# Kernel optimization log

Measured on AMD Instinct MI355X. Metric: run time of the kernel, lower is better.

The kernel has to match this reference:

```python
import jax, jax.numpy as jnp
import numpy as np

D = 1024
H = 16
DK = D // H
TB = 64  # temporal_bias_dim
SCALE = DK ** -0.5


def setup_inputs() -> dict:
    key = jax.random.key(0)
    ks = jax.random.split(key, 12)
    B, S = 8, 512
    s = 0.02
    return {
        "x": jax.random.normal(ks[0], (B, S, D), jnp.float32),
        "padding_masks": jnp.ones((B, 1, 1, S), jnp.int32),
        "batch_temporal_mat": jax.random.uniform(ks[1], (B, S, S), jnp.float32) * 100.0,
        "wq": jax.random.normal(ks[2], (D, D), jnp.float32) * s,
        "bq": jnp.zeros((D,), jnp.float32),
        "wk": jax.random.normal(ks[3], (D, D), jnp.float32) * s,
        "bk": jnp.zeros((D,), jnp.float32),
        "wv": jax.random.normal(ks[4], (D, D), jnp.float32) * s,
        "bv": jnp.zeros((D,), jnp.float32),
        "w_proj": jax.random.normal(ks[5], (D, D), jnp.float32) * s,
        "b_proj": jnp.zeros((D,), jnp.float32),
        "w_tb1": jax.random.normal(ks[6], (1, TB), jnp.float32) * 0.5,
        "b_tb1": jnp.zeros((TB,), jnp.float32),
        "w_tb2": jax.random.normal(ks[7], (TB, 1), jnp.float32) * 0.5,
        "b_tb2": jnp.zeros((1,), jnp.float32),
    }


def reference(x, padding_masks, batch_temporal_mat, wq, bq, wk, bk, wv, bv,
              w_proj, b_proj, w_tb1, b_tb1, w_tb2, b_tb2):
    B, S, _ = x.shape

    def heads(w, b):
        return (x @ w + b).reshape(B, S, H, DK).transpose(0, 2, 1, 3)  # (B,H,S,DK)

    q, k, v = heads(wq, bq), heads(wk, bk), heads(wv, bv)
    scores = jnp.einsum("bhqd,bhkd->bhqk", q, k) * SCALE  # (B,H,S,S)

    # temporal bias: 1/log(e + t) -> Linear(1,64) -> leaky_relu(0.2) -> Linear(64,1)
    t = 1.0 / jnp.log(jnp.exp(jnp.float32(1.0)) + batch_temporal_mat)  # (B,S,S)
    h = t[..., None] * w_tb1[0] + b_tb1  # (B,S,S,TB)
    h = jnp.where(h >= 0, h, 0.2 * h)
    bias = (h @ w_tb2)[..., 0] + b_tb2[0]  # (B,S,S)
    scores = scores + bias[:, None, :, :]

    neg_inf = jnp.float32(-jnp.inf)
    scores = jnp.where(padding_masks == 0, neg_inf, scores)
    causal = jnp.triu(jnp.ones((S, S), bool), k=1)  # (S,S), add_cls=False
    scores = jnp.where(causal[None, None], neg_inf, scores)

    p_attn = jax.nn.softmax(scores, axis=-1)
    out = jnp.einsum("bhqk,bhkd->bhqd", p_attn, v)
    out = out.transpose(0, 2, 1, 3).reshape(B, S, D)
    out = out @ w_proj + b_proj
    return out
```

## Files before the change

kernel.cpp:

```cpp
#include <hip/hip_runtime.h>
#include <hip/hip_bf16.h>

#define B_  8
#define S_  512
#define D_  1024
#define H_  16
#define DK_ 64
#define TB_ 64
#define SCALE_ 0.125f

typedef __attribute__((ext_vector_type(8))) short          bh8;
typedef __attribute__((ext_vector_type(4))) float          f32x4;
typedef __attribute__((ext_vector_type(8))) unsigned short us8;

__device__ __forceinline__ unsigned short f2bf(float f) {
    unsigned u = __float_as_uint(f);
    unsigned r = 0x7fffu + ((u >> 16) & 1u);
    return (unsigned short)((u + r) >> 16);
}

__global__ __launch_bounds__(256)
void cvt_x_kernel(const float* __restrict__ in, unsigned short* __restrict__ out, int n8)
{
    int i = blockIdx.x * 256 + threadIdx.x;
    if (i >= n8) return;
    float4 a = *(const float4*)&in[(size_t)i * 8];
    float4 b = *(const float4*)&in[(size_t)i * 8 + 4];
    us8 o;
    o[0] = f2bf(a.x); o[1] = f2bf(a.y); o[2] = f2bf(a.z); o[3] = f2bf(a.w);
    o[4] = f2bf(b.x); o[5] = f2bf(b.y); o[6] = f2bf(b.z); o[7] = f2bf(b.w);
    *(us8*)&out[(size_t)i * 8] = o;
}

__global__ __launch_bounds__(256)
void cvt_wt_kernel(const float* __restrict__ W, unsigned short* __restrict__ Wt)
{
    __shared__ float t[64][65];
    const int bx = blockIdx.x, by = blockIdx.y;
    const int c  = threadIdx.x & 63;
    const int r0 = threadIdx.x >> 6;
    #pragma unroll
    for (int i = 0; i < 16; ++i) {
        int r = r0 + i * 4;
        t[r][c] = W[(size_t)(by * 64 + r) * 1024 + bx * 64 + c];
    }
    __syncthreads();
    #pragma unroll
    for (int i = 0; i < 16; ++i) {
        int r = r0 + i * 4;
        Wt[(size_t)(bx * 64 + r) * 1024 + by * 64 + c] = f2bf(t[c][r]);
    }
}

template<int MODE>
__global__ __launch_bounds__(256)
void gemm_bf16_kernel(const unsigned short* __restrict__ A,
                      const unsigned short* __restrict__ Bt,
                      const float* __restrict__ bias,
                      float* __restrict__ C, unsigned short* __restrict__ Cb)
{
    __shared__ unsigned short As[128][72];
    __shared__ unsigned short Bs[128][72];
    const int tid  = threadIdx.x;
    const int lane = tid & 63;
    const int wid  = tid >> 6;
    const int wr   = wid >> 1, wc = wid & 1;
    const int row0 = blockIdx.x * 128;
    const int col0 = blockIdx.y * 128;

    f32x4 acc[4][4] = {};

    const int ur = tid >> 3;
    const int uc = (tid & 7) * 8;
    const int fr = lane & 15;
    const int fk = (lane >> 4) * 8;

    for (int k0 = 0; k0 < 1024; k0 += 64) {
        __syncthreads();
        #pragma unroll
        for (int i = 0; i < 4; ++i) {
            int r = ur + i * 32;
            *(int4*)&As[r][uc] = *(const int4*)&A [(size_t)(row0 + r) * 1024 + k0 + uc];
            *(int4*)&Bs[r][uc] = *(const int4*)&Bt[(size_t)(col0 + r) * 1024 + k0 + uc];
        }
        __syncthreads();
        #pragma unroll
        for (int ks = 0; ks < 2; ++ks) {
            bh8 af[4], bfr[4];
            #pragma unroll
            for (int r = 0; r < 4; ++r)
                af[r]  = *(const bh8*)&As[wr * 64 + r * 16 + fr][ks * 32 + fk];
            #pragma unroll
            for (int c = 0; c < 4; ++c)
                bfr[c] = *(const bh8*)&Bs[wc * 64 + c * 16 + fr][ks * 32 + fk];
            #pragma unroll
            for (int r = 0; r < 4; ++r)
                #pragma unroll
                for (int c = 0; c < 4; ++c)
                    acc[r][c] = __builtin_amdgcn_mfma_f32_16x16x32_bf16(
                        af[r], bfr[c], acc[r][c], 0, 0, 0);
        }
    }

    #pragma unroll
    for (int r = 0; r < 4; ++r) {
        #pragma unroll
        for (int c = 0; c < 4; ++c) {
            int n = col0 + wc * 64 + c * 16 + (lane & 15);
            float bn = bias[n];
            #pragma unroll
            for (int j = 0; j < 4; ++j) {
                int m = row0 + wr * 64 + r * 16 + (lane >> 4) * 4 + j;
                float o = acc[r][c][j] + bn;
                if (MODE == 0) {
                    C[(size_t)m * 1024 + n] = o;
                } else {
                    int bb = m >> 9, ss = m & 511;
                    int hh = n >> 6, dd = n & 63;
                    if (MODE == 1)
                        Cb[((size_t)((bb * H_ + hh) * S_ + ss)) * DK_ + dd] = f2bf(o);
                    else
                        Cb[((size_t)((bb * H_ + hh) * DK_ + dd)) * S_ + ss] = f2bf(o);
                }
            }
        }
    }
}

__global__ __launch_bounds__(256)
void tbias_kernel(const float* __restrict__ tm, const int* __restrict__ pmask,
                  const float* __restrict__ w1, const float* __restrict__ b1,
                  const float* __restrict__ w2, const float* __restrict__ b2,
                  float* __restrict__ bias)
{
    __shared__ float sw1[TB_], sb1[TB_], sw2[TB_];
    if (threadIdx.x < TB_) {
        sw1[threadIdx.x] = w1[threadIdx.x];
        sb1[threadIdx.x] = b1[threadIdx.x];
        sw2[threadIdx.x] = w2[threadIdx.x];
    }
    __syncthreads();
    const float ec  = 2.7182818284590452f;
    const float b2v = b2[0];
    const int n = B_ * S_ * S_;
    for (int i = blockIdx.x * blockDim.x + threadIdx.x; i < n;
         i += gridDim.x * blockDim.x) {
        int bb = i >> 18;
        int jj = i & (S_ - 1);
        float t   = 1.0f / logf(ec + tm[i]);
        float acc = b2v;
        #pragma unroll
        for (int j = 0; j < TB_; ++j) {
            float h = fmaf(t, sw1[j], sb1[j]);
            h = (h >= 0.f) ? h : 0.2f * h;
            acc = fmaf(h, sw2[j], acc);
        }
        bias[i] = (pmask[bb * S_ + jj] == 0) ? -1e30f : acc;
    }
}

__global__ __launch_bounds__(256)
void attn_kernel(const unsigned short* __restrict__ q,
                 const unsigned short* __restrict__ k,
                 const unsigned short* __restrict__ vt,
                 const float* __restrict__ biasm,
                 unsigned short* __restrict__ outb)
{
    __shared__ unsigned short Kl[64][72];
    __shared__ unsigned short Vl[64][72];
    __shared__ unsigned short Pl[64][72];

    const int tid  = threadIdx.x;
    const int lane = tid & 63;
    const int w    = tid >> 6;
    const int qt   = blockIdx.x;
    const int h    = blockIdx.y;
    const int b    = blockIdx.z;
    const int q0   = qt * 64;

    const int l15 = lane & 15;
    const int g   = lane >> 4;

    const size_t hb  = (size_t)(b * H_ + h) * S_;
    const unsigned short* kbase  = k  + hb * DK_;
    const unsigned short* vtbase = vt + ((size_t)(b * H_ + h) * DK_) * S_;

    const int qrow_a = q0 + w * 16 + l15;
    bh8 aq0 = *(const bh8*)&q[(hb + qrow_a) * DK_ +      g * 8];
    bh8 aq1 = *(const bh8*)&q[(hb + qrow_a) * DK_ + 32 + g * 8];

    const int qd = q0 + w * 16 + g * 4;

    f32x4 acc_o[4] = {};
    float m_run[4] = { -1e30f, -1e30f, -1e30f, -1e30f };
    float l_run[4] = {};

    for (int kt = 0; kt <= qt; ++kt) {
        __syncthreads();
        #pragma unroll
        for (int s = 0; s < 2; ++s) {
            int u  = tid + s * 256;
            int r  = u >> 3;
            int c8 = (u & 7) * 8;
            *(int4*)&Kl[r][c8] = *(const int4*)&kbase [(size_t)(kt * 64 + r) * DK_ + c8];
            *(int4*)&Vl[r][c8] = *(const int4*)&vtbase[(size_t)r * S_ + kt * 64 + c8];
        }
        __syncthreads();

        f32x4 sc[4];
        #pragma unroll
        for (int c = 0; c < 4; ++c) {
            bh8 bk0 = *(const bh8*)&Kl[c * 16 + l15][     g * 8];
            bh8 bk1 = *(const bh8*)&Kl[c * 16 + l15][32 + g * 8];
            f32x4 z = {};
            z = __builtin_amdgcn_mfma_f32_16x16x32_bf16(aq0, bk0, z, 0, 0, 0);
            sc[c] = __builtin_amdgcn_mfma_f32_16x16x32_bf16(aq1, bk1, z, 0, 0, 0);
        }

        float sv[4][4];
        #pragma unroll
        for (int j = 0; j < 4; ++j) {
            const float* br = biasm + ((size_t)b * S_ + qd + j) * S_ + kt * 64;
            #pragma unroll
            for (int c = 0; c < 4; ++c)
                sv[c][j] = fmaf(sc[c][j], SCALE_, br[c * 16 + l15]);
        }
        if (kt == qt) {
            #pragma unroll
            for (int c = 0; c < 4; ++c) {
                int kloc = c * 16 + l15;
                #pragma unroll
                for (int j = 0; j < 4; ++j)
                    if (kloc > w * 16 + g * 4 + j) sv[c][j] = -1e30f;
            }
        }

        #pragma unroll
        for (int j = 0; j < 4; ++j) {
            float mt = fmaxf(fmaxf(sv[0][j], sv[1][j]), fmaxf(sv[2][j], sv[3][j]));
            mt = fmaxf(mt, __shfl_xor(mt, 1));
            mt = fmaxf(mt, __shfl_xor(mt, 2));
            mt = fmaxf(mt, __shfl_xor(mt, 4));
            mt = fmaxf(mt, __shfl_xor(mt, 8));
            float m_new = fmaxf(m_run[j], mt);
            float resc  = __expf(m_run[j] - m_new);
            float psum  = 0.f;
            #pragma unroll
            for (int c = 0; c < 4; ++c) {
                float p = __expf(sv[c][j] - m_new);
                Pl[w * 16 + g * 4 + j][c * 16 + l15] = f2bf(p);
                psum += p;
            }
            psum += __shfl_xor(psum, 1);
            psum += __shfl_xor(psum, 2);
            psum += __shfl_xor(psum, 4);
            psum += __shfl_xor(psum, 8);
            l_run[j] = l_run[j] * resc + psum;
            m_run[j] = m_new;
            acc_o[0][j] *= resc; acc_o[1][j] *= resc;
            acc_o[2][j] *= resc; acc_o[3][j] *= resc;
        }

        asm volatile("s_waitcnt lgkmcnt(0)" ::: "memory");

        bh8 ap0 = *(const bh8*)&Pl[w * 16 + l15][     g * 8];
        bh8 ap1 = *(const bh8*)&Pl[w * 16 + l15][32 + g * 8];
        #pragma unroll
        for (int c2 = 0; c2 < 4; ++c2) {
            bh8 bv0 = *(const bh8*)&Vl[c2 * 16 + l15][     g * 8];
            bh8 bv1 = *(const bh8*)&Vl[c2 * 16 + l15][32 + g * 8];
            acc_o[c2] = __builtin_amdgcn_mfma_f32_16x16x32_bf16(ap0, bv0, acc_o[c2], 0, 0, 0);
            acc_o[c2] = __builtin_amdgcn_mfma_f32_16x16x32_bf16(ap1, bv1, acc_o[c2], 0, 0, 0);
        }
    }

    #pragma unroll
    for (int j = 0; j < 4; ++j) {
        float linv = 1.f / l_run[j];
        #pragma unroll
        for (int c2 = 0; c2 < 4; ++c2)
            outb[((size_t)(b * S_ + qd + j)) * D_ + h * DK_ + c2 * 16 + l15] =
                f2bf(acc_o[c2][j] * linv);
    }
}

extern "C" void kernel_launch(void* const* d_in, const int* in_sizes, int n_in,
                              void* d_out, int out_size, void* d_ws, size_t ws_size,
                              hipStream_t stream)
{
    const float* x     = (const float*)d_in[0];
    const int*   pm    = (const int*)  d_in[1];
    const float* tm    = (const float*)d_in[2];
    const float* wq    = (const float*)d_in[3];
    const float* bq    = (const float*)d_in[4];
    const float* wk    = (const float*)d_in[5];
    const float* bk    = (const float*)d_in[6];
    const float* wv    = (const float*)d_in[7];
    const float* bv    = (const float*)d_in[8];
    const float* wp    = (const float*)d_in[9];
    const float* bp    = (const float*)d_in[10];
    const float* w_tb1 = (const float*)d_in[11];
    const float* b_tb1 = (const float*)d_in[12];
    const float* w_tb2 = (const float*)d_in[13];
    const float* b_tb2 = (const float*)d_in[14];

    char* wsb = (char*)d_ws;
    const size_t MB = 1u << 20;
    unsigned short* xb  = (unsigned short*)wsb;
    unsigned short* wtq = (unsigned short*)(wsb + 8  * MB);
    unsigned short* wtk = wtq + 1048576;
    unsigned short* wtv = wtk + 1048576;
    unsigned short* wtp = wtv + 1048576;
    unsigned short* qw  = (unsigned short*)(wsb + 16 * MB);
    unsigned short* kw  = (unsigned short*)(wsb + 24 * MB);
    unsigned short* vtw = (unsigned short*)(wsb + 32 * MB);
    float*          bw  = (float*)        (wsb + 40 * MB);

    cvt_x_kernel<<<2048, 256, 0, stream>>>(x, xb, 524288);
    dim3 gw(16, 16);
    cvt_wt_kernel<<<gw, 256, 0, stream>>>(wq, wtq);
    cvt_wt_kernel<<<gw, 256, 0, stream>>>(wk, wtk);
    cvt_wt_kernel<<<gw, 256, 0, stream>>>(wv, wtv);
    cvt_wt_kernel<<<gw, 256, 0, stream>>>(wp, wtp);

    dim3 gg(32, 8);
    gemm_bf16_kernel<1><<<gg, 256, 0, stream>>>(xb, wtq, bq, nullptr, qw);
    gemm_bf16_kernel<1><<<gg, 256, 0, stream>>>(xb, wtk, bk, nullptr, kw);
    gemm_bf16_kernel<2><<<gg, 256, 0, stream>>>(xb, wtv, bv, nullptr, vtw);

    tbias_kernel<<<2048, 256, 0, stream>>>(tm, pm, w_tb1, b_tb1, w_tb2, b_tb2, bw);

    dim3 ga(8, H_, B_);
    attn_kernel<<<ga, 256, 0, stream>>>(qw, kw, vtw, bw, xb );

    gemm_bf16_kernel<0><<<gg, 256, 0, stream>>>(xb, wtp, bp, (float*)d_out, nullptr);
}
```

Measured before the change: 262.9 us.

## Fuse QKV GEMMs into one launch, shrink GEMM tiles, remap attention blocks

The three Q/K/V projection GEMMs become a single launch over a concatenated transposed weight buffer. Each block picks its bias and output layout from its column range. GEMM tiles shrink from 128x128 to 128x64, so the QKV grid has 1536 blocks and the projection grid 512, which gives more blocks per CU on the many-CU device. The attention launch becomes a 1D grid with a swizzled block-to-(b,h,qt) mapping so that consecutive blocks land on different XCDs, which may improve L2 locality for K/V. The smaller tiles reload A more often in exchange for better occupancy and less wave quantisation.

```diff
diff --git a/kernel.cpp b/kernel.cpp
--- a/kernel.cpp
+++ b/kernel.cpp
@@ -52,76 +52,153 @@
     }
 }
 
-template<int MODE>
-__global__ __launch_bounds__(256)
-void gemm_bf16_kernel(const unsigned short* __restrict__ A,
-                      const unsigned short* __restrict__ Bt,
-                      const float* __restrict__ bias,
-                      float* __restrict__ C, unsigned short* __restrict__ Cb)
+__global__ __launch_bounds__(256)
+void gemm_qkv_kernel(const unsigned short* __restrict__ A,
+                     const unsigned short* __restrict__ Wt,
+                     const float* __restrict__ bq, const float* __restrict__ bk,
+                     const float* __restrict__ bv,
+                     unsigned short* __restrict__ qo,
+                     unsigned short* __restrict__ ko,
+                     unsigned short* __restrict__ vo)
 {
     __shared__ unsigned short As[128][72];
-    __shared__ unsigned short Bs[128][72];
+    __shared__ unsigned short Bs[64][72];
     const int tid  = threadIdx.x;
     const int lane = tid & 63;
     const int wid  = tid >> 6;
     const int wr   = wid >> 1, wc = wid & 1;
     const int row0 = blockIdx.x * 128;
-    const int col0 = blockIdx.y * 128;
-
-    f32x4 acc[4][4] = {};
+    const int col0 = blockIdx.y * 64;
+
+    f32x4 acc[4][2] = {};
 
     const int ur = tid >> 3;
     const int uc = (tid & 7) * 8;
     const int fr = lane & 15;
     const int fk = (lane >> 4) * 8;
+    const int g  = lane >> 4;
 
     for (int k0 = 0; k0 < 1024; k0 += 64) {
         __syncthreads();
         #pragma unroll
         for (int i = 0; i < 4; ++i) {
             int r = ur + i * 32;
-            *(int4*)&As[r][uc] = *(const int4*)&A [(size_t)(row0 + r) * 1024 + k0 + uc];
-            *(int4*)&Bs[r][uc] = *(const int4*)&Bt[(size_t)(col0 + r) * 1024 + k0 + uc];
+            *(int4*)&As[r][uc] = *(const int4*)&A[(size_t)(row0 + r) * 1024 + k0 + uc];
+        }
+        #pragma unroll
+        for (int i = 0; i < 2; ++i) {
+            int r = ur + i * 32;
+            *(int4*)&Bs[r][uc] = *(const int4*)&Wt[(size_t)(col0 + r) * 1024 + k0 + uc];
         }
         __syncthreads();
         #pragma unroll
         for (int ks = 0; ks < 2; ++ks) {
-            bh8 af[4], bfr[4];
+            bh8 af[4], bfr[2];
             #pragma unroll
             for (int r = 0; r < 4; ++r)
                 af[r]  = *(const bh8*)&As[wr * 64 + r * 16 + fr][ks * 32 + fk];
             #pragma unroll
-            for (int c = 0; c < 4; ++c)
-                bfr[c] = *(const bh8*)&Bs[wc * 64 + c * 16 + fr][ks * 32 + fk];
+            for (int c = 0; c < 2; ++c)
+                bfr[c] = *(const bh8*)&Bs[wc * 32 + c * 16 + fr][ks * 32 + fk];
             #pragma unroll
             for (int r = 0; r < 4; ++r)
                 #pragma unroll
-                for (int c = 0; c < 4; ++c)
+                for (int c = 0; c < 2; ++c)
                     acc[r][c] = __builtin_amdgcn_mfma_f32_16x16x32_bf16(
                         af[r], bfr[c], acc[r][c], 0, 0, 0);
         }
     }
 
+    const int nh = col0 >> 10;
+    const float* bsel = (nh == 0) ? bq : (nh == 1) ? bk : bv;
+    unsigned short* outp = (nh == 0) ? qo : (nh == 1) ? ko : vo;
+
     #pragma unroll
     for (int r = 0; r < 4; ++r) {
         #pragma unroll
-        for (int c = 0; c < 4; ++c) {
-            int n = col0 + wc * 64 + c * 16 + (lane & 15);
+        for (int c = 0; c < 2; ++c) {
+            int n  = col0 + wc * 32 + c * 16 + (lane & 15);
+            int nn = n & 1023;
+            float bn = bsel[nn];
+            int hh = nn >> 6, dd = nn & 63;
+            #pragma unroll
+            for (int j = 0; j < 4; ++j) {
+                int m = row0 + wr * 64 + r * 16 + g * 4 + j;
+                float o = acc[r][c][j] + bn;
+                int bb = m >> 9, ss = m & 511;
+                if (nh == 2)
+                    outp[((size_t)((bb * H_ + hh) * DK_ + dd)) * S_ + ss] = f2bf(o);
+                else
+                    outp[((size_t)((bb * H_ + hh) * S_ + ss)) * DK_ + dd] = f2bf(o);
+            }
+        }
+    }
+}
+
+__global__ __launch_bounds__(256)
+void gemm_proj_kernel(const unsigned short* __restrict__ A,
+                      const unsigned short* __restrict__ Wt,
+                      const float* __restrict__ bias,
+                      float* __restrict__ C)
+{
+    __shared__ unsigned short As[128][72];
+    __shared__ unsigned short Bs[64][72];
+    const int tid  = threadIdx.x;
+    const int lane = tid & 63;
+    const int wid  = tid >> 6;
+    const int wr   = wid >> 1, wc = wid & 1;
+    const int row0 = blockIdx.x * 128;
+    const int col0 = blockIdx.y * 64;
+
+    f32x4 acc[4][2] = {};
+
+    const int ur = tid >> 3;
+    const int uc = (tid & 7) * 8;
+    const int fr = lane & 15;
+    const int fk = (lane >> 4) * 8;
+    const int g  = lane >> 4;
+
+    for (int k0 = 0; k0 < 1024; k0 += 64) {
+        __syncthreads();
+        #pragma unroll
+        for (int i = 0; i < 4; ++i) {
+            int r = ur + i * 32;
+            *(int4*)&As[r][uc] = *(const int4*)&A[(size_t)(row0 + r) * 1024 + k0 + uc];
+        }
+        #pragma unroll
+        for (int i = 0; i < 2; ++i) {
+            int r = ur + i * 32;
+            *(int4*)&Bs[r][uc] = *(const int4*)&Wt[(size_t)(col0 + r) * 1024 + k0 + uc];
+        }
+        __syncthreads();
+        #pragma unroll
+        for (int ks = 0; ks < 2; ++ks) {
+            bh8 af[4], bfr[2];
+            #pragma unroll
+            for (int r = 0; r < 4; ++r)
+                af[r]  = *(const bh8*)&As[wr * 64 + r * 16 + fr][ks * 32 + fk];
+            #pragma unroll
+            for (int c = 0; c < 2; ++c)
+                bfr[c] = *(const bh8*)&Bs[wc * 32 + c * 16 + fr][ks * 32 + fk];
+            #pragma unroll
+            for (int r = 0; r < 4; ++r)
+                #pragma unroll
+                for (int c = 0; c < 2; ++c)
+                    acc[r][c] = __builtin_amdgcn_mfma_f32_16x16x32_bf16(
+                        af[r], bfr[c], acc[r][c], 0, 0, 0);
+        }
+    }
+
+    #pragma unroll
+    for (int r = 0; r < 4; ++r) {
+        #pragma unroll
+        for (int c = 0; c < 2; ++c) {
+            int n = col0 + wc * 32 + c * 16 + (lane & 15);
             float bn = bias[n];
             #pragma unroll
             for (int j = 0; j < 4; ++j) {
-                int m = row0 + wr * 64 + r * 16 + (lane >> 4) * 4 + j;
-                float o = acc[r][c][j] + bn;
-                if (MODE == 0) {
-                    C[(size_t)m * 1024 + n] = o;
-                } else {
-                    int bb = m >> 9, ss = m & 511;
-                    int hh = n >> 6, dd = n & 63;
-                    if (MODE == 1)
-                        Cb[((size_t)((bb * H_ + hh) * S_ + ss)) * DK_ + dd] = f2bf(o);
-                    else
-                        Cb[((size_t)((bb * H_ + hh) * DK_ + dd)) * S_ + ss] = f2bf(o);
-                }
+                int m = row0 + wr * 64 + r * 16 + g * 4 + j;
+                C[(size_t)m * 1024 + n] = acc[r][c][j] + bn;
             }
         }
     }
@@ -173,10 +250,11 @@
     const int tid  = threadIdx.x;
     const int lane = tid & 63;
     const int w    = tid >> 6;
-    const int qt   = blockIdx.x;
-    const int h    = blockIdx.y;
-    const int b    = blockIdx.z;
-    const int q0   = qt * 64;
+    const int lin = (blockIdx.x & 7) * 128 + (blockIdx.x >> 3);
+    const int h   = lin & 15;
+    const int qt  = (lin >> 4) & 7;
+    const int b   = lin >> 7;
+    const int q0  = qt * 64;
 
     const int l15 = lane & 15;
     const int g   = lane >> 4;
@@ -306,32 +384,28 @@
 
     char* wsb = (char*)d_ws;
     const size_t MB = 1u << 20;
-    unsigned short* xb  = (unsigned short*)wsb;
-    unsigned short* wtq = (unsigned short*)(wsb + 8  * MB);
-    unsigned short* wtk = wtq + 1048576;
-    unsigned short* wtv = wtk + 1048576;
-    unsigned short* wtp = wtv + 1048576;
-    unsigned short* qw  = (unsigned short*)(wsb + 16 * MB);
-    unsigned short* kw  = (unsigned short*)(wsb + 24 * MB);
-    unsigned short* vtw = (unsigned short*)(wsb + 32 * MB);
-    float*          bw  = (float*)        (wsb + 40 * MB);
+    unsigned short* xb   = (unsigned short*)wsb;
+    unsigned short* wqkv = (unsigned short*)(wsb + 8  * MB);
+    unsigned short* wtp  = (unsigned short*)(wsb + 14 * MB);
+    unsigned short* qw   = (unsigned short*)(wsb + 16 * MB);
+    unsigned short* kw   = (unsigned short*)(wsb + 24 * MB);
+    unsigned short* vtw  = (unsigned short*)(wsb + 32 * MB);
+    float*          bw   = (float*)        (wsb + 40 * MB);
 
     cvt_x_kernel<<<2048, 256, 0, stream>>>(x, xb, 524288);
     dim3 gw(16, 16);
-    cvt_wt_kernel<<<gw, 256, 0, stream>>>(wq, wtq);
-    cvt_wt_kernel<<<gw, 256, 0, stream>>>(wk, wtk);
-    cvt_wt_kernel<<<gw, 256, 0, stream>>>(wv, wtv);
+    cvt_wt_kernel<<<gw, 256, 0, stream>>>(wq, wqkv);
+    cvt_wt_kernel<<<gw, 256, 0, stream>>>(wk, wqkv + 1048576);
+    cvt_wt_kernel<<<gw, 256, 0, stream>>>(wv, wqkv + 2097152);
     cvt_wt_kernel<<<gw, 256, 0, stream>>>(wp, wtp);
 
-    dim3 gg(32, 8);
-    gemm_bf16_kernel<1><<<gg, 256, 0, stream>>>(xb, wtq, bq, nullptr, qw);
-    gemm_bf16_kernel<1><<<gg, 256, 0, stream>>>(xb, wtk, bk, nullptr, kw);
-    gemm_bf16_kernel<2><<<gg, 256, 0, stream>>>(xb, wtv, bv, nullptr, vtw);
+    dim3 gqkv(32, 48);
+    gemm_qkv_kernel<<<gqkv, 256, 0, stream>>>(xb, wqkv, bq, bk, bv, qw, kw, vtw);
 
     tbias_kernel<<<2048, 256, 0, stream>>>(tm, pm, w_tb1, b_tb1, w_tb2, b_tb2, bw);
 
-    dim3 ga(8, H_, B_);
-    attn_kernel<<<ga, 256, 0, stream>>>(qw, kw, vtw, bw, xb );
-
-    gemm_bf16_kernel<0><<<gg, 256, 0, stream>>>(xb, wtp, bp, (float*)d_out, nullptr);
-}
+    attn_kernel<<<1024, 256, 0, stream>>>(qw, kw, vtw, bw, xb );
+
+    dim3 gp(32, 16);
+    gemm_proj_kernel<<<gp, 256, 0, stream>>>(xb, wtp, bp, (float*)d_out);
+}
```

Measured after the change: 229.1 us. 1.15x faster.
